# Kernel tuning notes

Hardware: AMD Instinct MI355X
Metric: run time of the kernel (lower is better)

## Reference

```python
import jax, jax.numpy as jnp
import numpy as np

N = 200000      # tweet nodes
E = 1600000     # edges
U = 20000       # users (num_users)
D = 64          # embedding_dimension1 == embedding_dimension2
NUMP, CATP = 20, 12
EPS = 0.1       # PyG FAConv default eps


def setup_inputs() -> dict:
    key = jax.random.key(0)
    ks = jax.random.split(key, 20)
    s = 0.05
    offs = jnp.sort(jax.random.randint(ks[3], (U + 1,), 0, N, dtype=jnp.int64))
    offs = offs.at[0].set(0).at[-1].set(N)
    return {
        "num_prop": jax.random.normal(ks[0], (N, NUMP), jnp.float32),
        "cat_prop": jax.random.normal(ks[1], (N, CATP), jnp.float32),
        "tweet_offsets": offs,
        "edge_index": jax.random.randint(ks[2], (2, E), 0, N, dtype=jnp.int64),
        "re_index": jax.random.randint(ks[4], (U,), 0, U, dtype=jnp.int64),
        "W_num": jax.random.normal(ks[5], (NUMP, D // 2), jnp.float32) * s,
        "b_num": jnp.zeros((D // 2,), jnp.float32),
        "W_cat": jax.random.normal(ks[6], (CATP, D // 2), jnp.float32) * s,
        "b_cat": jnp.zeros((D // 2,), jnp.float32),
        "W_tog": jax.random.normal(ks[7], (D, D), jnp.float32) * s,
        "b_tog": jnp.zeros((D,), jnp.float32),
        "att_l": jax.random.normal(ks[8], (D,), jnp.float32) * s,
        "att_r": jax.random.normal(ks[9], (D,), jnp.float32) * s,
        "W_f1": jax.random.normal(ks[10], (D, D // 2), jnp.float32) * s,
        "b_f1": jnp.zeros((D // 2,), jnp.float32),
        "W_lab": jax.random.normal(ks[11], (D // 2, 2), jnp.float32) * s,
        "b_lab": jnp.zeros((2,), jnp.float32),
    }


def reference(num_prop, cat_prop, tweet_offsets, edge_index, re_index,
              W_num, b_num, W_cat, b_cat, W_tog, b_tog,
              att_l, att_r, W_f1, b_f1, W_lab, b_lab):
    n = num_prop.shape[0]
    lrelu = jax.nn.leaky_relu  # slope 0.01, matches nn.LeakyReLU default

    num = lrelu(num_prop @ W_num + b_num)
    cat = lrelu(cat_prop @ W_cat + b_cat)
    x = lrelu(jnp.concatenate([num, cat], axis=1) @ W_tog + b_tog)  # [N, D]

    # gcn_norm with self-loops (PyG FAConv default normalize=True, add_self_loops=True)
    loop = jnp.arange(n, dtype=edge_index.dtype)
    src = jnp.concatenate([edge_index[0], loop])
    dst = jnp.concatenate([edge_index[1], loop])
    deg = jax.ops.segment_sum(jnp.ones(src.shape[0], jnp.float32), dst, num_segments=n)
    dinv = jnp.where(deg > 0, deg ** -0.5, 0.0)
    norm = dinv[src] * dinv[dst]  # [E+N]

    def faconv(h, h0):
        # alpha_e = tanh(att_l . h[src] + att_r . h[dst]); out_i = sum_e norm_e * alpha_e * h[src_e]
        al = h @ att_l
        ar = h @ att_r
        alpha = jnp.tanh(al[src] + ar[dst]) * norm
        agg = jax.ops.segment_sum(h[src] * alpha[:, None], dst, num_segments=n)
        return agg + EPS * h0

    x1 = faconv(x, x)      # dropout is identity in eval mode
    x2 = faconv(x1, x)
    x2 = jnp.sqrt(x2 ** 2 + 1e-8)

    # ragged per-user segment sum from CSR offsets (replaces python loop+slice)
    nseg = tweet_offsets.shape[0] - 1
    seg = jnp.searchsorted(tweet_offsets, jnp.arange(n), side='right') - 1
    seg = jnp.clip(seg, 0, nseg - 1)
    x3 = jax.ops.segment_sum(x2, seg, num_segments=nseg)  # [U, D]

    x3 = x3[re_index]
    h = lrelu(x3 @ W_f1 + b_f1)
    return h @ W_lab + b_lab
```

## Files before the change

kernel.cpp:

```cpp
#include <hip/hip_runtime.h>
#include <hip/hip_bf16.h>

#define LRELU(v) ((v) > 0.0f ? (v) : 0.01f * (v))
#define EPS 0.1f

#define BSHIFT  9
#define BSIZE   512
#define BIN_EPB 2048
#define BIN_CAP 6144
#define CAPP    10240

typedef __attribute__((ext_vector_type(8))) short bf16x8;
typedef __attribute__((ext_vector_type(4))) float f32x4;

__device__ __forceinline__ float fast_tanh(float v)
{
    float e = __expf(2.0f * v);
    return 1.0f - 2.0f * __builtin_amdgcn_rcpf(e + 1.0f);
}

__device__ __forceinline__ float bf2f(unsigned short h)
{
    return __uint_as_float(((unsigned int)h) << 16);
}
__device__ __forceinline__ unsigned short f2bf(float f)
{
    unsigned int u = __float_as_uint(f);
    u += 0x7FFFu + ((u >> 16) & 1u);
    return (unsigned short)(u >> 16);
}

__global__ void k_prep(const float* __restrict__ W_num, const float* __restrict__ W_cat,
                       const float* __restrict__ W_tog,
                       unsigned short* __restrict__ Wb, unsigned short* __restrict__ Wb1)
{
    int t = threadIdx.x;
    for (int i = t; i < 8 * 512; i += 256) {
        int tile = i >> 9;
        int kt   = tile >> 2, nt = tile & 3;
        int lane = (i >> 3) & 63;
        int j    = i & 7;
        int k    = kt * 32 + (lane >> 4) * 8 + j;
        int n    = nt * 16 + (lane & 15);
        Wb[i] = f2bf(W_tog[k * 64 + n]);
    }
    for (int i = t; i < 4 * 512; i += 256) {
        int nt   = i >> 9;
        int lane = (i >> 3) & 63;
        int j    = i & 7;
        int k    = (lane >> 4) * 8 + j;
        int n    = nt * 16 + (lane & 15);
        float w;
        if (n < 32) w = (k < 20)  ? W_num[k * 32 + n]              : 0.0f;
        else        w = (k >= 20) ? W_cat[(k - 20) * 32 + (n - 32)] : 0.0f;
        Wb1[i] = f2bf(w);
    }
}

__global__ void __launch_bounds__(256)
k_feat(const float* __restrict__ num_prop,
       const float* __restrict__ cat_prop,
       const unsigned short* __restrict__ Wb1,
       const float* __restrict__ b_num, const float* __restrict__ b_cat,
       const unsigned short* __restrict__ Wb, const float* __restrict__ b_tog,
       const float* __restrict__ att_l, const float* __restrict__ att_r,
       unsigned short* __restrict__ xb,
       float* __restrict__ al, float* __restrict__ ar, int N)
{
    __shared__ unsigned short in_lds[64][40];
    __shared__ unsigned short mid[64][72];

    int tid  = threadIdx.x;
    int lane = tid & 63;
    int w    = tid >> 6;
    int blockStart = blockIdx.x * 64;

    for (int i = tid; i < 64 * 20; i += 256) {
        int node = i / 20, k = i % 20;
        int n = min(blockStart + node, N - 1);
        in_lds[node][k] = f2bf(num_prop[(size_t)n * 20 + k]);
    }
    for (int i = tid; i < 64 * 12; i += 256) {
        int node = i / 12, k = i % 12;
        int n = min(blockStart + node, N - 1);
        in_lds[node][20 + k] = f2bf(cat_prop[(size_t)n * 12 + k]);
    }
    __syncthreads();

    int q   = lane >> 4;
    int c16 = lane & 15;

    bf16x8 ain = *(const bf16x8*)&in_lds[w * 16 + c16][q * 8];
    #pragma unroll
    for (int nt = 0; nt < 4; nt++) {
        bf16x8 b = *(const bf16x8*)&Wb1[nt * 512 + lane * 8];
        f32x4 acc = {0.0f, 0.0f, 0.0f, 0.0f};
        acc = __builtin_amdgcn_mfma_f32_16x16x32_bf16(ain, b, acc, 0, 0, 0);
        int   ch   = nt * 16 + c16;
        float bias = (ch < 32) ? b_num[ch] : b_cat[ch - 32];
        #pragma unroll
        for (int r = 0; r < 4; r++) {
            float s = acc[r] + bias;
            s = LRELU(s);
            mid[w * 16 + q * 4 + r][ch] = f2bf(s);
        }
    }

    bf16x8 a0 = *(const bf16x8*)&mid[w * 16 + c16][q * 8];
    bf16x8 a1 = *(const bf16x8*)&mid[w * 16 + c16][32 + q * 8];

    float pal[4] = {0, 0, 0, 0};
    float par[4] = {0, 0, 0, 0};

    #pragma unroll
    for (int nt = 0; nt < 4; nt++) {
        bf16x8 b0 = *(const bf16x8*)&Wb[(0 * 4 + nt) * 512 + lane * 8];
        bf16x8 b1 = *(const bf16x8*)&Wb[(1 * 4 + nt) * 512 + lane * 8];
        f32x4 acc = {0.0f, 0.0f, 0.0f, 0.0f};
        acc = __builtin_amdgcn_mfma_f32_16x16x32_bf16(a0, b0, acc, 0, 0, 0);
        acc = __builtin_amdgcn_mfma_f32_16x16x32_bf16(a1, b1, acc, 0, 0, 0);

        int   ch  = nt * 16 + c16;
        float bt  = b_tog[ch];
        float atl = att_l[ch];
        float atr = att_r[ch];
        #pragma unroll
        for (int r = 0; r < 4; r++) {
            float s = acc[r] + bt;
            s = LRELU(s);
            int n = blockStart + w * 16 + q * 4 + r;
            if (n < N) xb[(size_t)n * 64 + ch] = f2bf(s);
            pal[r] = fmaf(s, atl, pal[r]);
            par[r] = fmaf(s, atr, par[r]);
        }
    }

    #pragma unroll
    for (int r = 0; r < 4; r++) {
        float pl = pal[r], pr = par[r];
        #pragma unroll
        for (int off = 8; off > 0; off >>= 1) {
            pl += __shfl_xor(pl, off);
            pr += __shfl_xor(pr, off);
        }
        int n = blockStart + w * 16 + q * 4 + r;
        if (c16 == 0 && n < N) { al[n] = pl; ar[n] = pr; }
    }
}

__global__ void k_bin(const int* __restrict__ src, const int* __restrict__ dst,
                      int* __restrict__ bucket_cnt,
                      int* __restrict__ buckets, int E, int NB)
{
    __shared__ int  hist[BSIZE];
    __shared__ int  lbase[BSIZE];
    __shared__ int  gbase[BSIZE];
    __shared__ int2 stage[BIN_EPB];

    int tid  = threadIdx.x;
    int base = blockIdx.x * BIN_EPB;

    hist[tid] = 0;
    __syncthreads();

    int s[4], d[4], rk[4];
    #pragma unroll
    for (int k = 0; k < 4; k++) {
        int e = base + k * BSIZE + tid;
        s[k] = -1;
        if (e < E) {
            s[k] = src[e];
            d[k] = dst[e];
            rk[k] = atomicAdd(&hist[d[k] >> BSHIFT], 1);
        }
    }
    __syncthreads();

    int v = hist[tid];
    lbase[tid] = v;
    __syncthreads();
    for (int off = 1; off < BSIZE; off <<= 1) {
        int t = (tid >= off) ? lbase[tid - off] : 0;
        __syncthreads();
        lbase[tid] += t;
        __syncthreads();
    }
    int incl = lbase[tid];
    __syncthreads();
    lbase[tid] = incl - v;
    if (tid < NB && v > 0) gbase[tid] = atomicAdd(&bucket_cnt[tid], v);
    __syncthreads();

    #pragma unroll
    for (int k = 0; k < 4; k++) {
        if (s[k] >= 0) {
            int b = d[k] >> BSHIFT;
            stage[lbase[b] + rk[k]] = make_int2(s[k], d[k]);
        }
    }
    __syncthreads();

    int tot = min(BIN_EPB, E - base);
    for (int i = tid; i < tot; i += BSIZE) {
        int2 p = stage[i];
        int b = p.y >> BSHIFT;
        buckets[(size_t)b * BIN_CAP + gbase[b] + (i - lbase[b])] =
            (p.x << BSHIFT) | (p.y & (BSIZE - 1));
    }
}

__global__ void __launch_bounds__(512)
k_build(const int* __restrict__ buckets, const int* __restrict__ bucket_cnt,
        const float* __restrict__ al, const int* __restrict__ offs,
        float2* __restrict__ ald1,
        int* __restrict__ deg, int* __restrict__ row_start, int* __restrict__ seg,
        int* __restrict__ srcs, int N, int U)
{
    __shared__ int stage[BIN_CAP];
    __shared__ int cnt[BSIZE];
    __shared__ int sc[BSIZE];
    __shared__ int cur[BSIZE];

    int b   = blockIdx.x;
    int tid = threadIdx.x;
    int ecnt = bucket_cnt[b];
    const int* bp = buckets + (size_t)b * BIN_CAP;

    cnt[tid] = 0;
    cur[tid] = 0;
    __syncthreads();

    for (int i = tid; i < ecnt; i += BSIZE) {
        int e = bp[i];
        stage[i] = e;
        atomicAdd(&cnt[e & (BSIZE - 1)], 1);
    }
    __syncthreads();

    int d = cnt[tid];
    int p = (d + 7) & ~7;
    sc[tid] = p;
    __syncthreads();
    for (int off = 1; off < BSIZE; off <<= 1) {
        int t = (tid >= off) ? sc[tid - off] : 0;
        __syncthreads();
        sc[tid] += t;
        __syncthreads();
    }
    int rstart = sc[tid] - p;

    int gb = b * CAPP;
    int n  = b * BSIZE + tid;
    if (n < N) {
        deg[n]       = d;
        row_start[n] = gb + rstart;
        for (int k = d; k < p + 0; k++) srcs[gb + rstart + k] = 0;
        float dv = 1.0f / sqrtf((float)d + 1.0f);
        ald1[n] = make_float2(al[n], dv);

        int lo = 0, hi = U;
        while (lo < hi) {
            int mid = (lo + hi) >> 1;
            if (offs[mid] <= n) lo = mid + 1; else hi = mid;
        }
        seg[n] = min(max(lo - 1, 0), U - 1);
    }
    __syncthreads();

    for (int i = tid; i < ecnt; i += BSIZE) {
        int e = stage[i];
        int r = e & (BSIZE - 1);
        int o = atomicAdd(&cur[r], 1);
        int rs = sc[r] - ((cnt[r] + 7) & ~7);
        srcs[gb + rs + o] = e >> BSHIFT;
    }
}

__global__ void k_gather1(const int* __restrict__ srcs,
                          const int* __restrict__ row_start, const int* __restrict__ deg,
                          const unsigned short* __restrict__ xb,
                          const float2* __restrict__ ald1, const float* __restrict__ ar,
                          const float* __restrict__ att_l, const float* __restrict__ att_r,
                          unsigned short* __restrict__ h1b, float2* __restrict__ ald2,
                          float* __restrict__ ar2, int N)
{
    int lane = threadIdx.x & 63;
    int c0   = __builtin_amdgcn_readfirstlane(blockIdx.x * 4 + (threadIdx.x >> 6)) * 4;
    if (c0 >= N) return;
    int nend = min(c0 + 4, N);

    float atl = att_l[lane];
    float atr = att_r[lane];

    for (int n = c0; n < nend; n++) {
        int    s0   = row_start[n];
        int    cnt  = deg[n];
        int    cntp = (cnt + 7) & ~7;
        float2 self = ald1[n];
        float  di   = self.y;
        float  arn  = ar[n];

        float acc = 0.0f;
        for (int jb = 0; jb < cntp; jb += 64) {
            float a = 0.0f;
            int   e = jb + lane;
            if (e < cnt) {
                int s = srcs[s0 + e];
                float2 as = ald1[s];
                a = fast_tanh(as.x + arn) * as.y * di;
            }
            int te = min(cntp - jb, 64);
            for (int j = 0; j < te; j += 8) {
                int sv[8]; float vv[8];
                #pragma unroll
                for (int t = 0; t < 8; t++) sv[t] = srcs[s0 + jb + j + t];
                #pragma unroll
                for (int t = 0; t < 8; t++) vv[t] = bf2f(xb[(size_t)sv[t] * 64 + lane]);
                #pragma unroll
                for (int t = 0; t < 8; t++) acc = fmaf(vv[t], __shfl(a, j + t), acc);
            }
        }

        float selfa = fast_tanh(self.x + arn) * di * di;
        float xnl   = bf2f(xb[(size_t)n * 64 + lane]);
        float v     = acc + (selfa + EPS) * xnl;

        float pl = v * atl;
        float pr = v * atr;
        #pragma unroll
        for (int off = 32; off > 0; off >>= 1) {
            pl += __shfl_down(pl, off);
            pr += __shfl_down(pr, off);
        }
        h1b[(size_t)n * 64 + lane] = f2bf(v);
        if (lane == 0) { ald2[n] = make_float2(pl, di); ar2[n] = pr; }
    }
}

__global__ void k_gather2(const int* __restrict__ srcs,
                          const int* __restrict__ row_start, const int* __restrict__ deg,
                          const unsigned short* __restrict__ h1b,
                          const unsigned short* __restrict__ xb,
                          const float2* __restrict__ ald2, const float* __restrict__ ar2,
                          const int* __restrict__ seg,
                          float* __restrict__ x3, int N)
{
    int lane = threadIdx.x & 63;
    int c0   = __builtin_amdgcn_readfirstlane(blockIdx.x * 4 + (threadIdx.x >> 6)) * 4;
    if (c0 >= N) return;
    int nend = min(c0 + 4, N);

    float uacc = 0.0f;
    int   useg = seg[c0];

    for (int n = c0; n < nend; n++) {
        int sg = seg[n];
        if (sg != useg) {
            atomicAdd(&x3[(size_t)useg * 64 + lane], uacc);
            uacc = 0.0f;
            useg = sg;
        }

        int    s0   = row_start[n];
        int    cnt  = deg[n];
        int    cntp = (cnt + 7) & ~7;
        float2 self = ald2[n];
        float  di   = self.y;
        float  arn  = ar2[n];

        float acc = 0.0f;
        for (int jb = 0; jb < cntp; jb += 64) {
            float a = 0.0f;
            int   e = jb + lane;
            if (e < cnt) {
                int s = srcs[s0 + e];
                float2 as = ald2[s];
                a = fast_tanh(as.x + arn) * as.y * di;
            }
            int te = min(cntp - jb, 64);
            for (int j = 0; j < te; j += 8) {
                int sv[8]; float vv[8];
                #pragma unroll
                for (int t = 0; t < 8; t++) sv[t] = srcs[s0 + jb + j + t];
                #pragma unroll
                for (int t = 0; t < 8; t++) vv[t] = bf2f(h1b[(size_t)sv[t] * 64 + lane]);
                #pragma unroll
                for (int t = 0; t < 8; t++) acc = fmaf(vv[t], __shfl(a, j + t), acc);
            }
        }

        float selfa = fast_tanh(self.x + arn) * di * di;
        float h1l   = bf2f(h1b[(size_t)n * 64 + lane]);
        float xnl   = bf2f(xb[(size_t)n * 64 + lane]);
        float v = acc + selfa * h1l + EPS * xnl;
        uacc += sqrtf(v * v + 1e-8f);
    }
    atomicAdd(&x3[(size_t)useg * 64 + lane], uacc);
}

__global__ void __launch_bounds__(256)
k_head(const float* __restrict__ x3, const int* __restrict__ re_index,
       const float* __restrict__ W_f1, const float* __restrict__ b_f1,
       const float* __restrict__ W_lab, const float* __restrict__ b_lab,
       float* __restrict__ out, int U)
{
    __shared__ float wf[64][32];
    __shared__ float wl[32][2];

    int tid = threadIdx.x;
    for (int i = tid; i < 64 * 32; i += 256) wf[i >> 5][i & 31] = W_f1[i];
    if (tid < 64) wl[tid >> 1][tid & 1] = W_lab[tid];
    __syncthreads();

    int u = blockIdx.x * blockDim.x + tid;
    if (u >= U) return;

    int r = re_index[u];
    const float* y = x3 + (size_t)r * 64;

    float s[32];
    #pragma unroll
    for (int j = 0; j < 32; j++) s[j] = b_f1[j];

    for (int k = 0; k < 64; k++) {
        float yk = y[k];
        #pragma unroll
        for (int j = 0; j < 32; j++) s[j] = fmaf(yk, wf[k][j], s[j]);
    }

    float o0 = b_lab[0], o1 = b_lab[1];
    #pragma unroll
    for (int j = 0; j < 32; j++) {
        float t = LRELU(s[j]);
        o0 = fmaf(t, wl[j][0], o0);
        o1 = fmaf(t, wl[j][1], o1);
    }
    out[(size_t)u * 2 + 0] = o0;
    out[(size_t)u * 2 + 1] = o1;
}

extern "C" void kernel_launch(void* const* d_in, const int* in_sizes, int n_in,
                              void* d_out, int out_size, void* d_ws, size_t ws_size,
                              hipStream_t stream)
{
    const float* num_prop = (const float*)d_in[0];
    const float* cat_prop = (const float*)d_in[1];
    const int*   offs     = (const int*)d_in[2];
    const int*   edge     = (const int*)d_in[3];
    const int*   re_index = (const int*)d_in[4];
    const float* W_num    = (const float*)d_in[5];
    const float* b_num    = (const float*)d_in[6];
    const float* W_cat    = (const float*)d_in[7];
    const float* b_cat    = (const float*)d_in[8];
    const float* W_tog    = (const float*)d_in[9];
    const float* b_tog    = (const float*)d_in[10];
    const float* att_l    = (const float*)d_in[11];
    const float* att_r    = (const float*)d_in[12];
    const float* W_f1     = (const float*)d_in[13];
    const float* b_f1     = (const float*)d_in[14];
    const float* W_lab    = (const float*)d_in[15];
    const float* b_lab    = (const float*)d_in[16];

    const int N = in_sizes[0] / 20;
    const int E = in_sizes[3] / 2;
    const int U = in_sizes[4];

    const int* src = edge;
    const int* dst = edge + E;

    const int NB = (N + BSIZE - 1) >> BSHIFT;

    float* ws = (float*)d_ws;
    size_t off = 0;
    unsigned short* xb  = (unsigned short*)(ws + off); off += (size_t)N * 32;
    unsigned short* h1b = (unsigned short*)(ws + off); off += (size_t)N * 32;
    float2* ald1 = (float2*)(ws + off); off += (size_t)N * 2;
    float2* ald2 = (float2*)(ws + off); off += (size_t)N * 2;
    int*    buckets = (int*)(ws + off); off += (size_t)NB * BIN_CAP;
    float*  al   = ws + off; off += N;
    float*  ar   = ws + off; off += N;
    float*  ar2  = ws + off; off += N;
    float*  x3   = ws + off; off += (size_t)U * 64;
    unsigned short* Wb  = (unsigned short*)(ws + off); off += 2048;
    unsigned short* Wb1 = (unsigned short*)(ws + off); off += 1024;
    int*    deg        = (int*)(ws + off); off += N;
    int*    row_start  = (int*)(ws + off); off += N;
    int*    seg        = (int*)(ws + off); off += N;
    int*    bucket_cnt = (int*)(ws + off); off += NB;
    int*    srcs       = (int*)(ws + off); off += (size_t)NB * CAPP;

    hipMemsetAsync(bucket_cnt, 0, (size_t)NB * 4, stream);
    hipMemsetAsync(x3, 0, (size_t)U * 64 * 4, stream);

    const int nbC   = (N + 15) / 16;
    const int nbBin = (E + BIN_EPB - 1) / BIN_EPB;

    k_prep<<<1, 256, 0, stream>>>(W_num, W_cat, W_tog, Wb, Wb1);

    k_feat<<<(N + 63) / 64, 256, 0, stream>>>(num_prop, cat_prop, Wb1, b_num, b_cat,
                                              Wb, b_tog, att_l, att_r, xb, al, ar, N);

    k_bin<<<nbBin, BSIZE, 0, stream>>>(src, dst, bucket_cnt, buckets, E, NB);

    k_build<<<NB, BSIZE, 0, stream>>>(buckets, bucket_cnt, al, offs, ald1,
                                      deg, row_start, seg, srcs, N, U);

    k_gather1<<<nbC, 256, 0, stream>>>(srcs, row_start, deg, xb, ald1, ar,
                                       att_l, att_r, h1b, ald2, ar2, N);

    k_gather2<<<nbC, 256, 0, stream>>>(srcs, row_start, deg, h1b, xb,
                                       ald2, ar2, seg, x3, N);

    k_head<<<(U + 255) / 256, 256, 0, stream>>>(x3, re_index, W_f1, b_f1, W_lab, b_lab,
                                                (float*)d_out, U);
}
```

Before: 327.3 us.

## Merge feature MLP and edge binning into one heterogeneous kernel launch

Fuses the independent k_feat and k_bin kernels into a single launch, with blockIdx deciding whether a block bins edges or computes node features. The feature path now uses 512-thread blocks covering 128 nodes each, and the two share one LDS buffer. The aim is to drop a launch and its inter-kernel drain so the memory-bound binning and the MFMA feature work can run on the GPU at the same time. The cost is a larger fixed LDS footprint (28 KB) for every block, which may reduce occupancy for the feature blocks.

```diff
diff --git a/kernel.cpp b/kernel.cpp
--- a/kernel.cpp
+++ b/kernel.cpp
@@ -57,155 +57,156 @@
     }
 }
 
-__global__ void __launch_bounds__(256)
-k_feat(const float* __restrict__ num_prop,
-       const float* __restrict__ cat_prop,
-       const unsigned short* __restrict__ Wb1,
-       const float* __restrict__ b_num, const float* __restrict__ b_cat,
-       const unsigned short* __restrict__ Wb, const float* __restrict__ b_tog,
-       const float* __restrict__ att_l, const float* __restrict__ att_r,
-       unsigned short* __restrict__ xb,
-       float* __restrict__ al, float* __restrict__ ar, int N)
-{
-    __shared__ unsigned short in_lds[64][40];
-    __shared__ unsigned short mid[64][72];
-
-    int tid  = threadIdx.x;
-    int lane = tid & 63;
-    int w    = tid >> 6;
-    int blockStart = blockIdx.x * 64;
-
-    for (int i = tid; i < 64 * 20; i += 256) {
-        int node = i / 20, k = i % 20;
-        int n = min(blockStart + node, N - 1);
-        in_lds[node][k] = f2bf(num_prop[(size_t)n * 20 + k]);
-    }
-    for (int i = tid; i < 64 * 12; i += 256) {
-        int node = i / 12, k = i % 12;
-        int n = min(blockStart + node, N - 1);
-        in_lds[node][20 + k] = f2bf(cat_prop[(size_t)n * 12 + k]);
-    }
-    __syncthreads();
-
-    int q   = lane >> 4;
-    int c16 = lane & 15;
-
-    bf16x8 ain = *(const bf16x8*)&in_lds[w * 16 + c16][q * 8];
-    #pragma unroll
-    for (int nt = 0; nt < 4; nt++) {
-        bf16x8 b = *(const bf16x8*)&Wb1[nt * 512 + lane * 8];
-        f32x4 acc = {0.0f, 0.0f, 0.0f, 0.0f};
-        acc = __builtin_amdgcn_mfma_f32_16x16x32_bf16(ain, b, acc, 0, 0, 0);
-        int   ch   = nt * 16 + c16;
-        float bias = (ch < 32) ? b_num[ch] : b_cat[ch - 32];
+__global__ void __launch_bounds__(512)
+k_featbin(
+          const float* __restrict__ num_prop, const float* __restrict__ cat_prop,
+          const unsigned short* __restrict__ Wb1, const float* __restrict__ b_num,
+          const float* __restrict__ b_cat, const unsigned short* __restrict__ Wb,
+          const float* __restrict__ b_tog, const float* __restrict__ att_l,
+          const float* __restrict__ att_r, unsigned short* __restrict__ xb,
+          float* __restrict__ al, float* __restrict__ ar,
+          const int* __restrict__ src, const int* __restrict__ dst,
+          int* __restrict__ bucket_cnt, int* __restrict__ buckets,
+          int nbBin, int N, int E, int NB)
+{
+    __shared__ __align__(16) char shmem[28672];
+
+    int tid = threadIdx.x;
+
+    if ((int)blockIdx.x < nbBin) {
+        int*  hist  = (int*)shmem;
+        int*  lbase = hist + BSIZE;
+        int*  gbase = lbase + BSIZE;
+        int2* stage = (int2*)(gbase + BSIZE);
+
+        int base = blockIdx.x * BIN_EPB;
+
+        hist[tid] = 0;
+        __syncthreads();
+
+        int s[4], d[4], rk[4];
+        #pragma unroll
+        for (int k = 0; k < 4; k++) {
+            int e = base + k * BSIZE + tid;
+            s[k] = -1;
+            if (e < E) {
+                s[k] = src[e];
+                d[k] = dst[e];
+                rk[k] = atomicAdd(&hist[d[k] >> BSHIFT], 1);
+            }
+        }
+        __syncthreads();
+
+        int v = hist[tid];
+        lbase[tid] = v;
+        __syncthreads();
+        for (int off = 1; off < BSIZE; off <<= 1) {
+            int t = (tid >= off) ? lbase[tid - off] : 0;
+            __syncthreads();
+            lbase[tid] += t;
+            __syncthreads();
+        }
+        int incl = lbase[tid];
+        __syncthreads();
+        lbase[tid] = incl - v;
+        if (tid < NB && v > 0) gbase[tid] = atomicAdd(&bucket_cnt[tid], v);
+        __syncthreads();
+
+        #pragma unroll
+        for (int k = 0; k < 4; k++) {
+            if (s[k] >= 0) {
+                int b = d[k] >> BSHIFT;
+                stage[lbase[b] + rk[k]] = make_int2(s[k], d[k]);
+            }
+        }
+        __syncthreads();
+
+        int tot = min(BIN_EPB, E - base);
+        for (int i = tid; i < tot; i += BSIZE) {
+            int2 p = stage[i];
+            int b = p.y >> BSHIFT;
+            buckets[(size_t)b * BIN_CAP + gbase[b] + (i - lbase[b])] =
+                (p.x << BSHIFT) | (p.y & (BSIZE - 1));
+        }
+    } else {
+        unsigned short (*in_lds)[40] = (unsigned short(*)[40])shmem;
+        unsigned short (*mid)[72]    = (unsigned short(*)[72])(shmem + 10240);
+
+        int lane = tid & 63;
+        int w    = tid >> 6;
+        int blockStart = (blockIdx.x - nbBin) * 128;
+
+        for (int i = tid; i < 128 * 20; i += 512) {
+            int node = i / 20, k = i % 20;
+            int n = min(blockStart + node, N - 1);
+            in_lds[node][k] = f2bf(num_prop[(size_t)n * 20 + k]);
+        }
+        for (int i = tid; i < 128 * 12; i += 512) {
+            int node = i / 12, k = i % 12;
+            int n = min(blockStart + node, N - 1);
+            in_lds[node][20 + k] = f2bf(cat_prop[(size_t)n * 12 + k]);
+        }
+        __syncthreads();
+
+        int q   = lane >> 4;
+        int c16 = lane & 15;
+
+        bf16x8 ain = *(const bf16x8*)&in_lds[w * 16 + c16][q * 8];
+        #pragma unroll
+        for (int nt = 0; nt < 4; nt++) {
+            bf16x8 b = *(const bf16x8*)&Wb1[nt * 512 + lane * 8];
+            f32x4 acc = {0.0f, 0.0f, 0.0f, 0.0f};
+            acc = __builtin_amdgcn_mfma_f32_16x16x32_bf16(ain, b, acc, 0, 0, 0);
+            int   ch   = nt * 16 + c16;
+            float bias = (ch < 32) ? b_num[ch] : b_cat[ch - 32];
+            #pragma unroll
+            for (int r = 0; r < 4; r++) {
+                float s = acc[r] + bias;
+                s = LRELU(s);
+                mid[w * 16 + q * 4 + r][ch] = f2bf(s);
+            }
+        }
+
+        bf16x8 a0 = *(const bf16x8*)&mid[w * 16 + c16][q * 8];
+        bf16x8 a1 = *(const bf16x8*)&mid[w * 16 + c16][32 + q * 8];
+
+        float pal[4] = {0, 0, 0, 0};
+        float par[4] = {0, 0, 0, 0};
+
+        #pragma unroll
+        for (int nt = 0; nt < 4; nt++) {
+            bf16x8 b0 = *(const bf16x8*)&Wb[(0 * 4 + nt) * 512 + lane * 8];
+            bf16x8 b1 = *(const bf16x8*)&Wb[(1 * 4 + nt) * 512 + lane * 8];
+            f32x4 acc = {0.0f, 0.0f, 0.0f, 0.0f};
+            acc = __builtin_amdgcn_mfma_f32_16x16x32_bf16(a0, b0, acc, 0, 0, 0);
+            acc = __builtin_amdgcn_mfma_f32_16x16x32_bf16(a1, b1, acc, 0, 0, 0);
+
+            int   ch  = nt * 16 + c16;
+            float bt  = b_tog[ch];
+            float atl = att_l[ch];
+            float atr = att_r[ch];
+            #pragma unroll
+            for (int r = 0; r < 4; r++) {
+                float s = acc[r] + bt;
+                s = LRELU(s);
+                int n = blockStart + w * 16 + q * 4 + r;
+                if (n < N) xb[(size_t)n * 64 + ch] = f2bf(s);
+                pal[r] = fmaf(s, atl, pal[r]);
+                par[r] = fmaf(s, atr, par[r]);
+            }
+        }
+
         #pragma unroll
         for (int r = 0; r < 4; r++) {
-            float s = acc[r] + bias;
-            s = LRELU(s);
-            mid[w * 16 + q * 4 + r][ch] = f2bf(s);
-        }
-    }
-
-    bf16x8 a0 = *(const bf16x8*)&mid[w * 16 + c16][q * 8];
-    bf16x8 a1 = *(const bf16x8*)&mid[w * 16 + c16][32 + q * 8];
-
-    float pal[4] = {0, 0, 0, 0};
-    float par[4] = {0, 0, 0, 0};
-
-    #pragma unroll
-    for (int nt = 0; nt < 4; nt++) {
-        bf16x8 b0 = *(const bf16x8*)&Wb[(0 * 4 + nt) * 512 + lane * 8];
-        bf16x8 b1 = *(const bf16x8*)&Wb[(1 * 4 + nt) * 512 + lane * 8];
-        f32x4 acc = {0.0f, 0.0f, 0.0f, 0.0f};
-        acc = __builtin_amdgcn_mfma_f32_16x16x32_bf16(a0, b0, acc, 0, 0, 0);
-        acc = __builtin_amdgcn_mfma_f32_16x16x32_bf16(a1, b1, acc, 0, 0, 0);
-
-        int   ch  = nt * 16 + c16;
-        float bt  = b_tog[ch];
-        float atl = att_l[ch];
-        float atr = att_r[ch];
-        #pragma unroll
-        for (int r = 0; r < 4; r++) {
-            float s = acc[r] + bt;
-            s = LRELU(s);
+            float pl = pal[r], pr = par[r];
+            #pragma unroll
+            for (int off = 8; off > 0; off >>= 1) {
+                pl += __shfl_xor(pl, off);
+                pr += __shfl_xor(pr, off);
+            }
             int n = blockStart + w * 16 + q * 4 + r;
-            if (n < N) xb[(size_t)n * 64 + ch] = f2bf(s);
-            pal[r] = fmaf(s, atl, pal[r]);
-            par[r] = fmaf(s, atr, par[r]);
-        }
-    }
-
-    #pragma unroll
-    for (int r = 0; r < 4; r++) {
-        float pl = pal[r], pr = par[r];
-        #pragma unroll
-        for (int off = 8; off > 0; off >>= 1) {
-            pl += __shfl_xor(pl, off);
-            pr += __shfl_xor(pr, off);
-        }
-        int n = blockStart + w * 16 + q * 4 + r;
-        if (c16 == 0 && n < N) { al[n] = pl; ar[n] = pr; }
-    }
-}
-
-__global__ void k_bin(const int* __restrict__ src, const int* __restrict__ dst,
-                      int* __restrict__ bucket_cnt,
-                      int* __restrict__ buckets, int E, int NB)
-{
-    __shared__ int  hist[BSIZE];
-    __shared__ int  lbase[BSIZE];
-    __shared__ int  gbase[BSIZE];
-    __shared__ int2 stage[BIN_EPB];
-
-    int tid  = threadIdx.x;
-    int base = blockIdx.x * BIN_EPB;
-
-    hist[tid] = 0;
-    __syncthreads();
-
-    int s[4], d[4], rk[4];
-    #pragma unroll
-    for (int k = 0; k < 4; k++) {
-        int e = base + k * BSIZE + tid;
-        s[k] = -1;
-        if (e < E) {
-            s[k] = src[e];
-            d[k] = dst[e];
-            rk[k] = atomicAdd(&hist[d[k] >> BSHIFT], 1);
-        }
-    }
-    __syncthreads();
-
-    int v = hist[tid];
-    lbase[tid] = v;
-    __syncthreads();
-    for (int off = 1; off < BSIZE; off <<= 1) {
-        int t = (tid >= off) ? lbase[tid - off] : 0;
-        __syncthreads();
-        lbase[tid] += t;
-        __syncthreads();
-    }
-    int incl = lbase[tid];
-    __syncthreads();
-    lbase[tid] = incl - v;
-    if (tid < NB && v > 0) gbase[tid] = atomicAdd(&bucket_cnt[tid], v);
-    __syncthreads();
-
-    #pragma unroll
-    for (int k = 0; k < 4; k++) {
-        if (s[k] >= 0) {
-            int b = d[k] >> BSHIFT;
-            stage[lbase[b] + rk[k]] = make_int2(s[k], d[k]);
-        }
-    }
-    __syncthreads();
-
-    int tot = min(BIN_EPB, E - base);
-    for (int i = tid; i < tot; i += BSIZE) {
-        int2 p = stage[i];
-        int b = p.y >> BSHIFT;
-        buckets[(size_t)b * BIN_CAP + gbase[b] + (i - lbase[b])] =
-            (p.x << BSHIFT) | (p.y & (BSIZE - 1));
+            if (c16 == 0 && n < N) { al[n] = pl; ar[n] = pr; }
+        }
     }
 }
 
@@ -254,7 +255,7 @@
     if (n < N) {
         deg[n]       = d;
         row_start[n] = gb + rstart;
-        for (int k = d; k < p + 0; k++) srcs[gb + rstart + k] = 0;
+        for (int k = d; k < p; k++) srcs[gb + rstart + k] = 0;
         float dv = 1.0f / sqrtf((float)d + 1.0f);
         ald1[n] = make_float2(al[n], dv);
 
@@ -492,15 +493,17 @@
     hipMemsetAsync(bucket_cnt, 0, (size_t)NB * 4, stream);
     hipMemsetAsync(x3, 0, (size_t)U * 64 * 4, stream);
 
-    const int nbC   = (N + 15) / 16;
-    const int nbBin = (E + BIN_EPB - 1) / BIN_EPB;
+    const int nbC    = (N + 15) / 16;
+    const int nbBin  = (E + BIN_EPB - 1) / BIN_EPB;
+    const int nbFeat = (N + 127) / 128;
 
     k_prep<<<1, 256, 0, stream>>>(W_num, W_cat, W_tog, Wb, Wb1);
 
-    k_feat<<<(N + 63) / 64, 256, 0, stream>>>(num_prop, cat_prop, Wb1, b_num, b_cat,
-                                              Wb, b_tog, att_l, att_r, xb, al, ar, N);
-
-    k_bin<<<nbBin, BSIZE, 0, stream>>>(src, dst, bucket_cnt, buckets, E, NB);
+    k_featbin<<<nbBin + nbFeat, 512, 0, stream>>>(num_prop, cat_prop, Wb1, b_num,
+                                                  b_cat, Wb, b_tog, att_l, att_r,
+                                                  xb, al, ar,
+                                                  src, dst, bucket_cnt, buckets,
+                                                  nbBin, N, E, NB);
 
     k_build<<<NB, BSIZE, 0, stream>>>(buckets, bucket_cnt, al, offs, ald1,
                                       deg, row_start, seg, srcs, N, U);
```

Measured after the change: 324.2 us. No clear change (-1.0%).
